# Kernel tuning notes

Hardware: AMD Instinct MI355X
Metric: run time of the kernel (lower is better)

The kernel has to match this reference:

```python
import jax, jax.numpy as jnp
import numpy as np

NHEADS = 8
HD = 64          # h_emb_dim = embed_dim // num_heads
IN_EMB_LEN = 5   # agent-aware: k_same, k_other, q_same, q_other, v
PAD = 1          # kernel_size // 2


def conv2d(x, w, b):
    y = jax.lax.conv_general_dilated(
        x, w, window_strides=(1, 1), padding=[(PAD, PAD), (PAD, PAD)],
        dimension_numbers=("NCHW", "OIHW", "NCHW"))
    return y + b[None, :, None, None]


def setup_inputs() -> dict:
    key = jax.random.key(0)
    ks = jax.random.split(key, 6)
    b, seq, c, h, w = 1, 384, 512, 8, 8
    inp = jax.random.normal(ks[0], (b, seq, c, h, w), dtype=jnp.float32)
    attn_mask = jax.random.normal(ks[1], (b * NHEADS, seq, seq), dtype=jnp.float32) * 0.1
    agent_aware_mask = jax.random.randint(ks[2], (b * NHEADS, seq, seq), 0, 2, dtype=jnp.int32)
    w_in = jax.random.normal(ks[3], (IN_EMB_LEN * c, c, 3, 3), dtype=jnp.float32) * 0.02
    b_in = jnp.zeros((IN_EMB_LEN * c,), dtype=jnp.float32)
    w_out = jax.random.normal(ks[4], (c, c, 3, 3), dtype=jnp.float32) * 0.02
    b_out = jnp.zeros((c,), dtype=jnp.float32)
    return {"inp": inp, "attn_mask": attn_mask, "agent_aware_mask": agent_aware_mask,
            "w_in": w_in, "b_in": b_in, "w_out": w_out, "b_out": b_out}


def reference(inp, attn_mask, agent_aware_mask, w_in, b_in, w_out, b_out):
    b, seq, c, h, w = inp.shape
    hw = h * w
    x = inp.reshape(b * seq, c, h, w)
    feats = conv2d(x, w_in, b_in)                      # [b*seq, 5*c, h, w]
    feats = feats.reshape(b, seq, IN_EMB_LEN * HD, NHEADS * hw)
    feats = jnp.transpose(feats, (0, 3, 1, 2)).reshape(b * NHEADS, hw, seq, IN_EMB_LEN * HD)
    k_same, k_other, q_same, q_other, v = jnp.split(feats, IN_EMB_LEN, axis=3)
    scale = 1.0 / jnp.sqrt(jnp.asarray(HD, dtype=feats.dtype))
    am = attn_mask[:, None]                            # [b*H, 1, seq, seq]
    s_same = jnp.einsum("bpqd,bpkd->bpqk", q_same * scale, k_same) + am
    s_other = jnp.einsum("bpqd,bpkd->bpqk", q_other * scale, k_other) + am
    a_same = jax.nn.softmax(s_same, axis=-1)
    a_other = jax.nn.softmax(s_other, axis=-1)
    m = agent_aware_mask.astype(feats.dtype)[:, None]  # [b*H, 1, seq, seq]
    attn = m * a_same + (1.0 - m) * a_other
    out = jnp.einsum("bpqk,bpkd->bpqd", attn, v)       # [b*H, hw, seq, HD]
    out = out.reshape(b, NHEADS * hw, seq, HD)
    out = jnp.transpose(out, (0, 2, 3, 1)).reshape(b * seq, c, h, w)
    out = conv2d(out, w_out, b_out)
    return out.reshape(b, seq, c, h, w)
```

## Files before the change

### kernel.cpp

```cpp
#include <hip/hip_runtime.h>
#include <stdint.h>
#include <stddef.h>

typedef __attribute__((ext_vector_type(4))) float floatx4;
typedef __attribute__((ext_vector_type(8))) short shortx8;
typedef __attribute__((ext_vector_type(4))) short shortx4;
typedef __attribute__((ext_vector_type(4))) _Float16 halfx4;

#define DEVI static __device__ __forceinline__

DEVI uint16_t f2bf(float f) {
  uint32_t u = __builtin_bit_cast(uint32_t, f);
  u += 0x7fffu + ((u >> 16) & 1u);
  return (uint16_t)(u >> 16);
}
DEVI float bf2f(uint16_t u) {
  return __builtin_bit_cast(float, (uint32_t)u << 16);
}

DEVI void gload_lds16(const void* g, void* lds) {
  unsigned int off = (unsigned int)(uintptr_t)lds;
  __builtin_amdgcn_global_load_lds(
      (const __attribute__((address_space(1))) unsigned int*)g,
      (__attribute__((address_space(3))) unsigned int*)off,
      16, 0, 0);
}


__global__ __launch_bounds__(256) void k_prep_x(const float* __restrict__ inp,
                                                uint16_t* __restrict__ Xb) {
  __shared__ float T[64 * 65];
  const int tid = threadIdx.x;
  const int t = blockIdx.x >> 3, cb = blockIdx.x & 7;
  const float* src = inp + ((size_t)t * 512 + cb * 64) * 64;
  {
    int ci = tid >> 2, so = (tid & 3) * 16;
#pragma unroll
    for (int j = 0; j < 4; ++j) {
      float4 v = *(const float4*)&src[ci * 64 + so + 4 * j];
      T[ci * 65 + so + 4 * j + 0] = v.x;
      T[ci * 65 + so + 4 * j + 1] = v.y;
      T[ci * 65 + so + 4 * j + 2] = v.z;
      T[ci * 65 + so + 4 * j + 3] = v.w;
    }
  }
  __syncthreads();
  {
    int s = tid >> 2, co = (tid & 3) * 16;
    uint16_t* dst = Xb + ((size_t)(t * 64 + s) * 512) + cb * 64 + co;
    shortx8 o0, o1;
#pragma unroll
    for (int j = 0; j < 8; ++j) o0[j] = (short)f2bf(T[(co + j) * 65 + s]);
#pragma unroll
    for (int j = 0; j < 8; ++j) o1[j] = (short)f2bf(T[(co + 8 + j) * 65 + s]);
    *(shortx8*)dst = o0;
    *(shortx8*)(dst + 8) = o1;
  }
}

__global__ __launch_bounds__(256) void k_prep_win(const float* __restrict__ w_in,
                                                  const float* __restrict__ b_in,
                                                  uint16_t* __restrict__ Wr,
                                                  float* __restrict__ bias_p) {
  __shared__ float B[4608];
  const int tid = threadIdx.x;
  const int cp = blockIdx.x;
  const int e = cp >> 9, h = (cp >> 6) & 7, d = cp & 63;
  const int co = e * 512 + d * 8 + h;
  const float* src = w_in + (size_t)co * 4608;
#pragma unroll
  for (int it = 0; it < 9; ++it) {
    int i2 = it * 256 + tid;
    *(float2*)&B[i2 * 2] = *(const float2*)&src[i2 * 2];
  }
  if (tid == 0) bias_p[cp] = b_in[co];
  __syncthreads();
  const int ci = tid * 2;
#pragma unroll
  for (int tap = 0; tap < 9; ++tap) {
    uint32_t pk = (uint32_t)f2bf(B[ci * 9 + tap]) |
                  ((uint32_t)f2bf(B[(ci + 1) * 9 + tap]) << 16);
    *(uint32_t*)&Wr[((size_t)tap * 2560 + cp) * 512 + ci] = pk;
  }
}

__global__ __launch_bounds__(256) void k_prep_wout(const float* __restrict__ w_out,
                                                   uint16_t* __restrict__ Wr) {
  __shared__ float B[4608];
  const int tid = threadIdx.x;
  const int co2 = blockIdx.x;
  const float* src = w_out + (size_t)co2 * 4608;
#pragma unroll
  for (int it = 0; it < 9; ++it) {
    int i2 = it * 256 + tid;
    *(float2*)&B[i2 * 2] = *(const float2*)&src[i2 * 2];
  }
  __syncthreads();
  const int c2 = tid * 2;
  const int oci0 = (c2 & 63) * 8 + (c2 >> 6);
  const int oci1 = ((c2 + 1) & 63) * 8 + ((c2 + 1) >> 6);
#pragma unroll
  for (int tap = 0; tap < 9; ++tap) {
    uint32_t pk = (uint32_t)f2bf(B[oci0 * 9 + tap]) |
                  ((uint32_t)f2bf(B[oci1 * 9 + tap]) << 16);
    *(uint32_t*)&Wr[((size_t)tap * 512 + co2) * 512 + c2] = pk;
  }
}

__global__ __launch_bounds__(256) void k_prep_mask(const float* __restrict__ am,
                                                   const int* __restrict__ gm,
                                                   float* __restrict__ amT,
                                                   uint8_t* __restrict__ gmT) {
  __shared__ float A_[64 * 65];
  __shared__ float G_[64 * 65];
  const int tid = threadIdx.x;
  const int b = blockIdx.x;
  const int h = b / 36, rr = b % 36;
  const int q0 = (rr / 6) * 64, k0 = (rr % 6) * 64;
  {
    int qr = tid >> 2, ko = (tid & 3) * 16;
    const float* ap = am + ((size_t)h * 384 + q0 + qr) * 384 + k0 + ko;
    const int* gp = gm + ((size_t)h * 384 + q0 + qr) * 384 + k0 + ko;
#pragma unroll
    for (int j = 0; j < 4; ++j) {
      float4 v = *(const float4*)(ap + 4 * j);
      int4 g = *(const int4*)(gp + 4 * j);
      int kk = ko + 4 * j;
      A_[(kk + 0) * 65 + qr] = v.x;
      A_[(kk + 1) * 65 + qr] = v.y;
      A_[(kk + 2) * 65 + qr] = v.z;
      A_[(kk + 3) * 65 + qr] = v.w;
      G_[(kk + 0) * 65 + qr] = (float)g.x;
      G_[(kk + 1) * 65 + qr] = (float)g.y;
      G_[(kk + 2) * 65 + qr] = (float)g.z;
      G_[(kk + 3) * 65 + qr] = (float)g.w;
    }
  }
  __syncthreads();
  {
    const float L2E = 1.44269504f;
    int kr = tid >> 2, qo = (tid & 3) * 16;
    float* aop = amT + ((size_t)h * 384 + k0 + kr) * 384 + q0 + qo;
    uint8_t* gop = gmT + ((size_t)h * 384 + k0 + kr) * 384 + q0 + qo;
    uint32_t gw[4];
#pragma unroll
    for (int j = 0; j < 4; ++j) {
      float4 o;
      o.x = A_[kr * 65 + qo + 4 * j + 0] * L2E - 8.0f;
      o.y = A_[kr * 65 + qo + 4 * j + 1] * L2E - 8.0f;
      o.z = A_[kr * 65 + qo + 4 * j + 2] * L2E - 8.0f;
      o.w = A_[kr * 65 + qo + 4 * j + 3] * L2E - 8.0f;
      *(float4*)(aop + 4 * j) = o;
      gw[j] = (uint32_t)(uint8_t)G_[kr * 65 + qo + 4 * j + 0] |
              ((uint32_t)(uint8_t)G_[kr * 65 + qo + 4 * j + 1] << 8) |
              ((uint32_t)(uint8_t)G_[kr * 65 + qo + 4 * j + 2] << 16) |
              ((uint32_t)(uint8_t)G_[kr * 65 + qo + 4 * j + 3] << 24);
    }
    uint4 gv = {gw[0], gw[1], gw[2], gw[3]};
    *(uint4*)gop = gv;
  }
}

template <int MTOT, int EPI>
__global__ __launch_bounds__(256) void conv_gemm(const uint16_t* __restrict__ W,
                                                 const uint16_t* __restrict__ X,
                                                 const float* __restrict__ bias,
                                                 uint16_t* __restrict__ Fo,
                                                 float* __restrict__ Oo) {
  __shared__ __attribute__((aligned(16))) uint16_t Wl[128 * 64];
  __shared__ __attribute__((aligned(16))) uint16_t Xl[128 * 64];

  const int tid = threadIdx.x;
  const int lane = tid & 63;
  const int wave = tid >> 6;
  const int quad = lane >> 4;
  const int l15 = lane & 15;
  const int wm = wave >> 1;
  const int wn = wave & 1;

  const int m_blk = blockIdx.x / 192;
  const int n_blk = blockIdx.x % 192;
  const int m0 = m_blk * 128;
  const long n0 = (long)n_blk * 128;

  const int srow = wave * 32 + (lane >> 3);
  const int spos = lane & 7;

  floatx4 acc[4][4];
#pragma unroll
  for (int i = 0; i < 4; ++i)
#pragma unroll
    for (int j = 0; j < 4; ++j) acc[i][j] = (floatx4)0.0f;

  int arow[4];
#pragma unroll
  for (int mt = 0; mt < 4; ++mt) arow[mt] = wm * 64 + mt * 16 + l15;

  for (int kc = 0; kc < 8; ++kc) {
    for (int tap = 0; tap < 9; ++tap) {
      __syncthreads();
      if (tap == 0) {
#pragma unroll
        for (int i = 0; i < 4; ++i) {
          int row = srow + i * 8;
          int c = spos ^ (row & 7);
          gload_lds16(X + ((n0 + row) * 512 + kc * 64 + c * 8),
                      Xl + row * 64 + spos * 8);
        }
      }
      {
        const uint16_t* wg = W + ((size_t)tap * MTOT + m0) * 512 + kc * 64;
#pragma unroll
        for (int i = 0; i < 4; ++i) {
          int row = srow + i * 8;
          int c = spos ^ (row & 7);
          gload_lds16(wg + (size_t)row * 512 + c * 8, Wl + row * 64 + spos * 8);
        }
      }
      __syncthreads();

      const int dy = tap / 3 - 1, dx = tap % 3 - 1;
      int brow[4];
      bool bok[4];
#pragma unroll
      for (int nt = 0; nt < 4; ++nt) {
        int s = nt * 16 + l15;
        int y = (s >> 3) + dy, x = (s & 7) + dx;
        bool ok = ((unsigned)y < 8u) && ((unsigned)x < 8u);
        bok[nt] = ok;
        brow[nt] = wn * 64 + (ok ? (y * 8 + x) : 0);
      }

#pragma unroll
      for (int ks = 0; ks < 2; ++ks) {
        shortx8 af[4], bf[4];
#pragma unroll
        for (int mt = 0; mt < 4; ++mt) {
          int pos = ((ks << 2) | quad) ^ (arow[mt] & 7);
          af[mt] = *(const shortx8*)(Wl + arow[mt] * 64 + pos * 8);
        }
#pragma unroll
        for (int nt = 0; nt < 4; ++nt) {
          int pos = ((ks << 2) | quad) ^ (brow[nt] & 7);
          shortx8 v = *(const shortx8*)(Xl + brow[nt] * 64 + pos * 8);
          bf[nt] = bok[nt] ? v : (shortx8)(short)0;
        }
#pragma unroll
        for (int mt = 0; mt < 4; ++mt)
#pragma unroll
          for (int nt = 0; nt < 4; ++nt)
            acc[mt][nt] = __builtin_amdgcn_mfma_f32_16x16x32_bf16(
                af[mt], bf[nt], acc[mt][nt], 0, 0, 0);
      }
    }
  }

  if (EPI == 0) {
#pragma unroll
    for (int mt = 0; mt < 4; ++mt) {
      int cpb = m0 + wm * 64 + mt * 16 + quad * 4;
      floatx4 bv = *(const floatx4*)(bias + cpb);
      int e = cpb >> 9, h = (cpb >> 6) & 7, d0 = cpb & 63;
#pragma unroll
      for (int nt = 0; nt < 4; ++nt) {
        long ng = n0 + wn * 64 + nt * 16 + l15;
        int t = (int)(ng >> 6), p = (int)(ng & 63);
        shortx4 pk;
#pragma unroll
        for (int r = 0; r < 4; ++r) pk[r] = (short)f2bf(acc[mt][nt][r] + bv[r]);
        *(shortx4*)(Fo + ((((size_t)(e * 8 + h) * 64 + p) * 384 + t) * 64 + d0)) = pk;
      }
    }
  } else {
#pragma unroll
    for (int mt = 0; mt < 4; ++mt) {
      int co = m0 + wm * 64 + mt * 16 + quad * 4;
      floatx4 bv = *(const floatx4*)(bias + co);
#pragma unroll
      for (int nt = 0; nt < 4; ++nt) {
        long ng = n0 + wn * 64 + nt * 16 + l15;
        int t = (int)(ng >> 6), s = (int)(ng & 63);
        float* op = Oo + ((size_t)t * 512 + co) * 64 + s;
#pragma unroll
        for (int r = 0; r < 4; ++r) op[(size_t)r * 64] = acc[mt][nt][r] + bv[r];
      }
    }
  }
}

__global__ __launch_bounds__(256) void attn_kernel(const uint16_t* __restrict__ F,
                                                   const float* __restrict__ amT,
                                                   const uint8_t* __restrict__ gmT,
                                                   uint16_t* __restrict__ G) {
  __shared__ __attribute__((aligned(16))) _Float16 Vt[64 * 392];

  const int tid = threadIdx.x;
  const int lane = tid & 63;
  const int wave = tid >> 6;
  const int quad = lane >> 4;
  const int l15 = lane & 15;

  const int qt = blockIdx.x % 6;
  const int hp = blockIdx.x / 6;
  const int h = hp >> 6, p = hp & 63;

  const size_t slab = (size_t)384 * 64;
  const uint16_t* Ks = F + ((size_t)(0 * 8 + h) * 64 + p) * slab;
  const uint16_t* Ko = F + ((size_t)(1 * 8 + h) * 64 + p) * slab;
  const uint16_t* Qs = F + ((size_t)(2 * 8 + h) * 64 + p) * slab;
  const uint16_t* Qo = F + ((size_t)(3 * 8 + h) * 64 + p) * slab;
  const uint16_t* Vv = F + ((size_t)(4 * 8 + h) * 64 + p) * slab;

  if (tid < 192) {
    const int kk0 = tid * 2;
    const uint16_t* v0 = Vv + (size_t)kk0 * 64;
#pragma unroll
    for (int dc = 0; dc < 8; ++dc) {
      shortx8 a = *(const shortx8*)(v0 + dc * 8);
      shortx8 b = *(const shortx8*)(v0 + 64 + dc * 8);
#pragma unroll
      for (int e = 0; e < 8; ++e) {
        _Float16 fa = (_Float16)bf2f((uint16_t)a[e]);
        _Float16 fb = (_Float16)bf2f((uint16_t)b[e]);
        uint32_t pk = (uint32_t)__builtin_bit_cast(uint16_t, fa) |
                      ((uint32_t)__builtin_bit_cast(uint16_t, fb) << 16);
        *(uint32_t*)&Vt[(dc * 8 + e) * 392 + kk0] = pk;
      }
    }
  }

  const int q0 = qt * 64 + wave * 16;
  shortx8 qsf[2], qof[2];
#pragma unroll
  for (int ks = 0; ks < 2; ++ks) {
    qsf[ks] = *(const shortx8*)(Qs + (size_t)(q0 + l15) * 64 + ks * 32 + quad * 8);
    qof[ks] = *(const shortx8*)(Qo + (size_t)(q0 + l15) * 64 + ks * 32 + quad * 8);
  }

  floatx4 Os[4], Oo[4];
#pragma unroll
  for (int i = 0; i < 4; ++i) { Os[i] = (floatx4)0.0f; Oo[i] = (floatx4)0.0f; }
  float ls = 0.f, lo = 0.f;

  const float C1 = 0.125f * 1.44269504f;

  __syncthreads();

  for (int kb = 0; kb < 6; ++kb) {
    const int k0 = kb * 64;

    const float* amr = amT + ((size_t)h * 384 + k0 + quad * 4) * 384 + q0 + l15;
    const uint8_t* gmr = gmT + ((size_t)h * 384 + k0 + quad * 4) * 384 + q0 + l15;
    float am[4][4];
    uint8_t gm[4][4];
#pragma unroll
    for (int nt = 0; nt < 4; ++nt)
#pragma unroll
      for (int r = 0; r < 4; ++r) {
        am[nt][r] = amr[((size_t)nt * 16 + r) * 384];
        gm[nt][r] = gmr[((size_t)nt * 16 + r) * 384];
      }

    floatx4 Ss[4], So[4];
#pragma unroll
    for (int nt = 0; nt < 4; ++nt) { Ss[nt] = (floatx4)0.0f; So[nt] = (floatx4)0.0f; }
#pragma unroll
    for (int nt = 0; nt < 4; ++nt) {
      const size_t krow = (size_t)(k0 + nt * 16 + l15) * 64;
#pragma unroll
      for (int ks = 0; ks < 2; ++ks) {
        shortx8 ka = *(const shortx8*)(Ks + krow + ks * 32 + quad * 8);
        Ss[nt] = __builtin_amdgcn_mfma_f32_16x16x32_bf16(ka, qsf[ks], Ss[nt], 0, 0, 0);
        shortx8 kb_ = *(const shortx8*)(Ko + krow + ks * 32 + quad * 8);
        So[nt] = __builtin_amdgcn_mfma_f32_16x16x32_bf16(kb_, qof[ks], So[nt], 0, 0, 0);
      }
    }

    halfx4 pbs[4], pbo[4];
#pragma unroll
    for (int kt = 0; kt < 4; ++kt)
#pragma unroll
      for (int r = 0; r < 4; ++r) {
        float ps = exp2f(Ss[kt][r] * C1 + am[kt][r]);
        float po = exp2f(So[kt][r] * C1 + am[kt][r]);
        ls += ps;
        lo += po;
        bool gb = gm[kt][r] != 0;
        pbs[kt][r] = gb ? (_Float16)ps : (_Float16)0.f;
        pbo[kt][r] = gb ? (_Float16)0.f : (_Float16)po;
      }

#pragma unroll
    for (int dt = 0; dt < 4; ++dt) {
      const _Float16* vrow = Vt + (size_t)(dt * 16 + l15) * 392 + k0;
#pragma unroll
      for (int kt = 0; kt < 4; ++kt) {
        halfx4 va = *(const halfx4*)(vrow + kt * 16 + quad * 4);
        Os[dt] = __builtin_amdgcn_mfma_f32_16x16x16f16(va, pbs[kt], Os[dt], 0, 0, 0);
        Oo[dt] = __builtin_amdgcn_mfma_f32_16x16x16f16(va, pbo[kt], Oo[dt], 0, 0, 0);
      }
    }
  }

  ls += __shfl_xor(ls, 16);
  ls += __shfl_xor(ls, 32);
  lo += __shfl_xor(lo, 16);
  lo += __shfl_xor(lo, 32);

  const float is = 1.f / ls, io = 1.f / lo;
  const int q = q0 + l15;
#pragma unroll
  for (int dt = 0; dt < 4; ++dt) {
    shortx4 pk;
#pragma unroll
    for (int r = 0; r < 4; ++r) pk[r] = (short)f2bf(Os[dt][r] * is + Oo[dt][r] * io);
    *(shortx4*)(G + ((size_t)q * 64 + p) * 512 + h * 64 + dt * 16 + quad * 4) = pk;
  }
}


extern "C" void kernel_launch(void* const* d_in, const int* in_sizes, int n_in,
                              void* d_out, int out_size, void* d_ws, size_t ws_size,
                              hipStream_t stream) {
  (void)in_sizes; (void)n_in; (void)out_size;

  const float* inp   = (const float*)d_in[0];
  const float* amask = (const float*)d_in[1];
  const int*   gmask = (const int*)d_in[2];
  const float* w_in  = (const float*)d_in[3];
  const float* b_in  = (const float*)d_in[4];
  const float* w_out = (const float*)d_in[5];
  const float* b_out = (const float*)d_in[6];
  float* out = (float*)d_out;

  const size_t SZ_WRIN  = (size_t)9 * 2560 * 512 * 2;
  const size_t SZ_WROUT = (size_t)9 * 512 * 512 * 2;
  const size_t SZ_BIAS  = 2560 * 4;
  const size_t SZ_XB    = (size_t)24576 * 512 * 2;
  const size_t SZ_F     = (size_t)5 * 8 * 64 * 384 * 64 * 2;
  if (ws_size < SZ_WRIN + SZ_WROUT + SZ_BIAS + SZ_XB + SZ_F) return;

  char* ws = (char*)d_ws;
  uint16_t* Wr_in  = (uint16_t*)ws;  ws += SZ_WRIN;
  uint16_t* Wr_out = (uint16_t*)ws;  ws += SZ_WROUT;
  float*    bias_p = (float*)ws;     ws += SZ_BIAS;
  uint16_t* Xb     = (uint16_t*)ws;  ws += SZ_XB;
  uint16_t* F      = (uint16_t*)ws;  ws += SZ_F;
  uint16_t* G      = Xb;
  float*    amT    = (float*)Wr_in;
  uint8_t*  gmT    = (uint8_t*)(amT + (size_t)8 * 384 * 384);

  k_prep_x<<<3072, 256, 0, stream>>>(inp, Xb);
  k_prep_win<<<2560, 256, 0, stream>>>(w_in, b_in, Wr_in, bias_p);
  k_prep_wout<<<512, 256, 0, stream>>>(w_out, Wr_out);
  conv_gemm<2560, 0><<<20 * 192, 256, 0, stream>>>(Wr_in, Xb, bias_p, F, nullptr);
  k_prep_mask<<<288, 256, 0, stream>>>(amask, gmask, amT, gmT);
  attn_kernel<<<512 * 6, 256, 0, stream>>>(F, amT, gmT, G);
  conv_gemm<512, 1><<<4 * 192, 256, 0, stream>>>(Wr_out, G, b_out, nullptr, out);
}
```

Before: 1.065 ms.

## Load conv weight fragments directly from global and drop per-tap LDS staging

The conv GEMM now keeps only the input tile in LDS and reads weight MFMA fragments straight from global memory into registers. This removes the per-tap LDS weight staging and both per-tap barriers, leaving one barrier pair per k-chunk. Out-of-bounds taps now index a zero-filled padding row in LDS instead of using a select. The trade-off is that each weight fragment is fetched by both N-waves from global/L2 with no LDS reuse, and global load latency is exposed directly in the MFMA loop.

```diff
diff --git a/kernel.cpp b/kernel.cpp
--- a/kernel.cpp
+++ b/kernel.cpp
@@ -167,8 +167,7 @@
                                                  const float* __restrict__ bias,
                                                  uint16_t* __restrict__ Fo,
                                                  float* __restrict__ Oo) {
-  __shared__ __attribute__((aligned(16))) uint16_t Wl[128 * 64];
-  __shared__ __attribute__((aligned(16))) uint16_t Xl[128 * 64];
+  __shared__ __attribute__((aligned(16))) uint16_t Xl[129 * 64];
 
   const int tid = threadIdx.x;
   const int lane = tid & 63;
@@ -186,64 +185,53 @@
   const int srow = wave * 32 + (lane >> 3);
   const int spos = lane & 7;
 
+  if (tid < 8) *(shortx8*)(Xl + 128 * 64 + tid * 8) = (shortx8)(short)0;
+
   floatx4 acc[4][4];
 #pragma unroll
   for (int i = 0; i < 4; ++i)
 #pragma unroll
     for (int j = 0; j < 4; ++j) acc[i][j] = (floatx4)0.0f;
 
-  int arow[4];
-#pragma unroll
-  for (int mt = 0; mt < 4; ++mt) arow[mt] = wm * 64 + mt * 16 + l15;
+  const uint16_t* aptr[4];
+#pragma unroll
+  for (int mt = 0; mt < 4; ++mt)
+    aptr[mt] = W + (size_t)(m0 + wm * 64 + mt * 16 + l15) * 512 + quad * 8;
 
   for (int kc = 0; kc < 8; ++kc) {
+    __syncthreads();
+#pragma unroll
+    for (int i = 0; i < 4; ++i) {
+      int row = srow + i * 8;
+      int c = spos ^ (row & 7);
+      gload_lds16(X + ((n0 + row) * 512 + kc * 64 + c * 8),
+                  Xl + row * 64 + spos * 8);
+    }
+    __syncthreads();
+
+#pragma unroll
     for (int tap = 0; tap < 9; ++tap) {
-      __syncthreads();
-      if (tap == 0) {
-#pragma unroll
-        for (int i = 0; i < 4; ++i) {
-          int row = srow + i * 8;
-          int c = spos ^ (row & 7);
-          gload_lds16(X + ((n0 + row) * 512 + kc * 64 + c * 8),
-                      Xl + row * 64 + spos * 8);
-        }
-      }
-      {
-        const uint16_t* wg = W + ((size_t)tap * MTOT + m0) * 512 + kc * 64;
-#pragma unroll
-        for (int i = 0; i < 4; ++i) {
-          int row = srow + i * 8;
-          int c = spos ^ (row & 7);
-          gload_lds16(wg + (size_t)row * 512 + c * 8, Wl + row * 64 + spos * 8);
-        }
-      }
-      __syncthreads();
-
       const int dy = tap / 3 - 1, dx = tap % 3 - 1;
       int brow[4];
-      bool bok[4];
 #pragma unroll
       for (int nt = 0; nt < 4; ++nt) {
         int s = nt * 16 + l15;
         int y = (s >> 3) + dy, x = (s & 7) + dx;
         bool ok = ((unsigned)y < 8u) && ((unsigned)x < 8u);
-        bok[nt] = ok;
-        brow[nt] = wn * 64 + (ok ? (y * 8 + x) : 0);
-      }
+        brow[nt] = ok ? (wn * 64 + y * 8 + x) : 128;
+      }
+      const size_t woff = (size_t)tap * MTOT * 512 + (size_t)kc * 64;
 
 #pragma unroll
       for (int ks = 0; ks < 2; ++ks) {
         shortx8 af[4], bf[4];
 #pragma unroll
-        for (int mt = 0; mt < 4; ++mt) {
-          int pos = ((ks << 2) | quad) ^ (arow[mt] & 7);
-          af[mt] = *(const shortx8*)(Wl + arow[mt] * 64 + pos * 8);
-        }
+        for (int mt = 0; mt < 4; ++mt)
+          af[mt] = *(const shortx8*)(aptr[mt] + woff + ks * 32);
 #pragma unroll
         for (int nt = 0; nt < 4; ++nt) {
           int pos = ((ks << 2) | quad) ^ (brow[nt] & 7);
-          shortx8 v = *(const shortx8*)(Xl + brow[nt] * 64 + pos * 8);
-          bf[nt] = bok[nt] ? v : (shortx8)(short)0;
+          bf[nt] = *(const shortx8*)(Xl + brow[nt] * 64 + pos * 8);
         }
 #pragma unroll
         for (int mt = 0; mt < 4; ++mt)
```

Measured after the change: 2.092 ms. +96.5%, slower.
